# Optimization experiments

Hardware: AMD Instinct MI355X
Metric: run time of the kernel (lower is better)

The kernel has to match this reference:

```python
import jax, jax.numpy as jnp
import numpy as np

NEG_SLOPE = 0.01  # nn.LeakyReLU default used in module

def leaky_relu(x):
    return jnp.where(x >= 0, x, NEG_SLOPE * x)

def setup_inputs() -> dict:
    key = jax.random.key(0)
    k1, k2, k3, k4, k5 = jax.random.split(key, 5)
    B, S, D, H, E = 4, 2048, 1024, 2048, 8
    s_in = 1.0 / np.sqrt(D)
    return {
        "inputs": jax.random.normal(k1, (B, S, D), dtype=jnp.float32),
        "Wg": jax.random.normal(k2, (E, D), dtype=jnp.float32) * s_in,
        "bg": jax.random.normal(k3, (E,), dtype=jnp.float32) * s_in,
        "We": jax.random.normal(k4, (E, H, D), dtype=jnp.float32) * s_in,
        "be": jax.random.normal(k5, (E, H), dtype=jnp.float32) * s_in,
    }

def reference(inputs, Wg, bg, We, be):
    # gate: [B,S,E]
    gate_logits = jnp.einsum('bsd,ed->bse', inputs, Wg) + bg
    gate_probs = jax.nn.softmax(gate_logits, axis=-1)
    # all experts densely: [B,S,E,H]
    expert_out = leaky_relu(jnp.einsum('bsd,ehd->bseh', inputs, We) + be)
    # gate-weighted reduction over experts: [B,S,H]
    weighted = jnp.einsum('bseh,bse->bsh', expert_out, gate_probs)
    return weighted
```

## Files before the change

kernel.cpp:

```cpp
#include <hip/hip_runtime.h>
#include <hip/hip_bf16.h>
#include <math.h>

#define M_TOK 8192
#define N_H   2048
#define K_D   1024
#define N_E   8

typedef __bf16 bf16x8 __attribute__((ext_vector_type(8)));
typedef __bf16 bf16x4 __attribute__((ext_vector_type(4)));
typedef float  f32x4  __attribute__((ext_vector_type(4)));

__device__ inline f32x4 mfma16(bf16x8 a, bf16x8 b, f32x4 c) {
  return __builtin_amdgcn_mfma_f32_16x16x32_bf16(a, b, c, 0, 0, 0);
}

__device__ inline void load16_lds(const void* g, void* l) {
  __builtin_amdgcn_global_load_lds(
      (const __attribute__((address_space(1))) void*)g,
      (__attribute__((address_space(3))) void*)l, 16, 0, 0);
}

__global__ __launch_bounds__(256) void cvt_kernel(const float* __restrict__ src,
                                                  __bf16* __restrict__ dst,
                                                  int n4) {
  int i = blockIdx.x * blockDim.x + threadIdx.x;
  const int stride = gridDim.x * blockDim.x;
  for (; i < n4; i += stride) {
    float4 v = ((const float4*)src)[i];
    bf16x4 o = {(__bf16)v.x, (__bf16)v.y, (__bf16)v.z, (__bf16)v.w};
    *(bf16x4*)(dst + (size_t)i * 4) = o;
  }
}

__global__ __launch_bounds__(256) void gate_kernel(const float* __restrict__ X,
                                                   const float* __restrict__ Wg,
                                                   const float* __restrict__ bg,
                                                   float* __restrict__ gate) {
  const int tid = threadIdx.x;
  const int lane = tid & 63;
  const int wv = tid >> 6;
  const int token = blockIdx.x * 4 + wv;
  const float* xrow = X + (size_t)token * K_D;

  float xr[16];
#pragma unroll
  for (int i = 0; i < 16; ++i) xr[i] = xrow[lane + i * 64];

  float l[N_E];
#pragma unroll
  for (int e = 0; e < N_E; ++e) {
    const float* wrow = Wg + e * K_D;
    float s = 0.f;
#pragma unroll
    for (int i = 0; i < 16; ++i) s += xr[i] * wrow[lane + i * 64];
#pragma unroll
    for (int off = 32; off > 0; off >>= 1) s += __shfl_xor(s, off);
    l[e] = s + bg[e];
  }
  float mx = l[0];
#pragma unroll
  for (int e = 1; e < N_E; ++e) mx = fmaxf(mx, l[e]);
  float p[N_E], den = 0.f;
#pragma unroll
  for (int e = 0; e < N_E; ++e) { p[e] = expf(l[e] - mx); den += p[e]; }
  const float inv = 1.f / den;
  if (lane == 0) {
#pragma unroll
    for (int e = 0; e < N_E; ++e) gate[(size_t)token * N_E + e] = p[e] * inv;
  }
}

__global__ __launch_bounds__(256, 2) void moe_main(
    const __bf16* __restrict__ Xb, const __bf16* __restrict__ Wb,
    const float* __restrict__ gate, const float* __restrict__ be,
    float* __restrict__ out) {
  __shared__ __bf16 As[128 * 32];
  __shared__ __bf16 Bs[128 * 32];
  __shared__ float gS[128 * 8];
  __shared__ float bS[8 * 128];

  const int tid = threadIdx.x;
  const int lane = tid & 63;
  const int wv = tid >> 6;
  const int wr = wv >> 1, wc = wv & 1;
  const int row0 = blockIdx.x * 128;
  const int col0 = blockIdx.y * 128;

  for (int i = tid; i < 1024; i += 256) {
    gS[i] = gate[(size_t)row0 * N_E + i];
    bS[i] = be[(size_t)(i >> 7) * N_H + col0 + (i & 127)];
  }

  const int rA = tid >> 2;
  const int kk = (tid & 3) * 8;
  const __bf16* aP0 = Xb + (size_t)(row0 + rA) * K_D + kk;
  const __bf16* aP1 = aP0 + (size_t)64 * K_D;

  const int lr = lane & 15;
  const int lk = (lane >> 4) * 8;
  const __bf16* aRd = &As[(wr * 64 + lr) * 32 + lk];
  const __bf16* bRd = &Bs[(wc * 64 + lr) * 32 + lk];

  f32x4 fin[4][4];
#pragma unroll
  for (int m = 0; m < 4; ++m)
#pragma unroll
    for (int n = 0; n < 4; ++n) fin[m][n] = (f32x4){0.f, 0.f, 0.f, 0.f};

  for (int e = 0; e < N_E; ++e) {
    const __bf16* bP0 =
        Wb + (size_t)e * N_H * K_D + (size_t)(col0 + rA) * K_D + kk;
    const __bf16* bP1 = bP0 + (size_t)64 * K_D;

    f32x4 acc[4][4];
#pragma unroll
    for (int m = 0; m < 4; ++m)
#pragma unroll
      for (int n = 0; n < 4; ++n) acc[m][n] = (f32x4){0.f, 0.f, 0.f, 0.f};

    for (int kt = 0; kt < K_D / 32; ++kt) {
      const int k0 = kt * 32;
      __syncthreads();
      load16_lds(aP0 + k0, &As[wv * 512]);
      load16_lds(aP1 + k0, &As[2048 + wv * 512]);
      load16_lds(bP0 + k0, &Bs[wv * 512]);
      load16_lds(bP1 + k0, &Bs[2048 + wv * 512]);
      __syncthreads();

      bf16x8 af[4], bfr[4];
#pragma unroll
      for (int m = 0; m < 4; ++m) af[m] = *(const bf16x8*)(aRd + m * 16 * 32);
#pragma unroll
      for (int n = 0; n < 4; ++n) bfr[n] = *(const bf16x8*)(bRd + n * 16 * 32);
#pragma unroll
      for (int m = 0; m < 4; ++m)
#pragma unroll
        for (int n = 0; n < 4; ++n)
          acc[m][n] = mfma16(af[m], bfr[n], acc[m][n]);
    }

#pragma unroll
    for (int m = 0; m < 4; ++m) {
#pragma unroll
      for (int j = 0; j < 4; ++j) {
        const int r = wr * 64 + m * 16 + (lane >> 4) * 4 + j;
        const float g = gS[r * 8 + e];
#pragma unroll
        for (int n = 0; n < 4; ++n) {
          float v = acc[m][n][j] + bS[e * 128 + wc * 64 + n * 16 + lr];
          v = (v >= 0.f) ? v : 0.01f * v;
          fin[m][n][j] += g * v;
        }
      }
    }
  }

#pragma unroll
  for (int m = 0; m < 4; ++m) {
#pragma unroll
    for (int j = 0; j < 4; ++j) {
      const size_t r = (size_t)(row0 + wr * 64 + m * 16 + (lane >> 4) * 4 + j);
#pragma unroll
      for (int n = 0; n < 4; ++n) {
        out[r * N_H + col0 + wc * 64 + n * 16 + lr] = fin[m][n][j];
      }
    }
  }
}

extern "C" void kernel_launch(void* const* d_in, const int* in_sizes, int n_in,
                              void* d_out, int out_size, void* d_ws, size_t ws_size,
                              hipStream_t stream) {
  const float* X  = (const float*)d_in[0];
  const float* Wg = (const float*)d_in[1];
  const float* bg = (const float*)d_in[2];
  const float* We = (const float*)d_in[3];
  const float* be = (const float*)d_in[4];
  float* out = (float*)d_out;

  char* ws = (char*)d_ws;
  __bf16* Xb   = (__bf16*)(ws);
  __bf16* Wb   = (__bf16*)(ws + (size_t)16 * 1024 * 1024);
  float*  gate = (float*)(ws + (size_t)48 * 1024 * 1024);

  cvt_kernel<<<2048, 256, 0, stream>>>(X, Xb, (M_TOK * K_D) / 4);
  cvt_kernel<<<2048, 256, 0, stream>>>(We, Wb, (N_E * N_H * K_D) / 4);

  gate_kernel<<<M_TOK / 4, 256, 0, stream>>>(X, Wg, bg, gate);

  dim3 grid(M_TOK / 128, N_H / 128);
  moe_main<<<grid, 256, 0, stream>>>(Xb, Wb, gate, be, out);
}
```

Before: 367.9 us.

## Process two experts per K-loop pass to reuse A tile and halve barriers

Restructures the expert loop so each K-sweep loads B tiles for two experts at once and computes both against the same A fragments. This halves the number of A tile loads and syncthreads pairs per block and doubles the MFMA work per barrier. In exchange the accumulator grows to 4x8 f32x4 per wave (128 extra VGPRs), which risks spills or lower occupancy under launch_bounds(256,2), and B shared memory doubles.

```diff
diff --git a/kernel.cpp b/kernel.cpp
--- a/kernel.cpp
+++ b/kernel.cpp
@@ -76,14 +76,14 @@
     const float* __restrict__ gate, const float* __restrict__ be,
     float* __restrict__ out) {
   __shared__ __bf16 As[128 * 32];
-  __shared__ __bf16 Bs[128 * 32];
+  __shared__ __bf16 Bs[256 * 32];
   __shared__ float gS[128 * 8];
   __shared__ float bS[8 * 128];
 
   const int tid = threadIdx.x;
   const int lane = tid & 63;
   const int wv = tid >> 6;
-  const int wr = wv >> 1, wc = wv & 1;
+  const int wr = wv >> 1, wn = wv & 1;
   const int row0 = blockIdx.x * 128;
   const int col0 = blockIdx.y * 128;
 
@@ -100,24 +100,27 @@
   const int lr = lane & 15;
   const int lk = (lane >> 4) * 8;
   const __bf16* aRd = &As[(wr * 64 + lr) * 32 + lk];
-  const __bf16* bRd = &Bs[(wc * 64 + lr) * 32 + lk];
+  const __bf16* bRd = &Bs[(wn * 64 + lr) * 32 + lk];
 
   f32x4 fin[4][4];
 #pragma unroll
   for (int m = 0; m < 4; ++m)
 #pragma unroll
-    for (int n = 0; n < 4; ++n) fin[m][n] = (f32x4){0.f, 0.f, 0.f, 0.f};
-
-  for (int e = 0; e < N_E; ++e) {
-    const __bf16* bP0 =
-        Wb + (size_t)e * N_H * K_D + (size_t)(col0 + rA) * K_D + kk;
-    const __bf16* bP1 = bP0 + (size_t)64 * K_D;
-
-    f32x4 acc[4][4];
+    for (int h = 0; h < 4; ++h) fin[m][h] = (f32x4){0.f, 0.f, 0.f, 0.f};
+
+  for (int p = 0; p < 4; ++p) {
+    const int e0 = p * 2;
+
+    const __bf16* bP0 = Wb + ((size_t)(e0 + 0) * N_H + col0 + 0  + rA) * K_D + kk;
+    const __bf16* bP1 = Wb + ((size_t)(e0 + 0) * N_H + col0 + 64 + rA) * K_D + kk;
+    const __bf16* bP2 = Wb + ((size_t)(e0 + 1) * N_H + col0 + 0  + rA) * K_D + kk;
+    const __bf16* bP3 = Wb + ((size_t)(e0 + 1) * N_H + col0 + 64 + rA) * K_D + kk;
+
+    f32x4 acc[4][8];
 #pragma unroll
     for (int m = 0; m < 4; ++m)
 #pragma unroll
-      for (int n = 0; n < 4; ++n) acc[m][n] = (f32x4){0.f, 0.f, 0.f, 0.f};
+      for (int n = 0; n < 8; ++n) acc[m][n] = (f32x4){0.f, 0.f, 0.f, 0.f};
 
     for (int kt = 0; kt < K_D / 32; ++kt) {
       const int k0 = kt * 32;
@@ -126,18 +129,21 @@
       load16_lds(aP1 + k0, &As[2048 + wv * 512]);
       load16_lds(bP0 + k0, &Bs[wv * 512]);
       load16_lds(bP1 + k0, &Bs[2048 + wv * 512]);
+      load16_lds(bP2 + k0, &Bs[4096 + wv * 512]);
+      load16_lds(bP3 + k0, &Bs[6144 + wv * 512]);
       __syncthreads();
 
-      bf16x8 af[4], bfr[4];
+      bf16x8 af[4];
 #pragma unroll
       for (int m = 0; m < 4; ++m) af[m] = *(const bf16x8*)(aRd + m * 16 * 32);
 #pragma unroll
-      for (int n = 0; n < 4; ++n) bfr[n] = *(const bf16x8*)(bRd + n * 16 * 32);
-#pragma unroll
-      for (int m = 0; m < 4; ++m)
-#pragma unroll
-        for (int n = 0; n < 4; ++n)
-          acc[m][n] = mfma16(af[m], bfr[n], acc[m][n]);
+      for (int n = 0; n < 8; ++n) {
+        const bf16x8 bfr =
+            *(const bf16x8*)(bRd + ((n >> 2) * 128 + (n & 3) * 16) * 32);
+#pragma unroll
+        for (int m = 0; m < 4; ++m)
+          acc[m][n] = mfma16(af[m], bfr, acc[m][n]);
+      }
     }
 
 #pragma unroll
@@ -145,12 +151,16 @@
 #pragma unroll
       for (int j = 0; j < 4; ++j) {
         const int r = wr * 64 + m * 16 + (lane >> 4) * 4 + j;
-        const float g = gS[r * 8 + e];
-#pragma unroll
-        for (int n = 0; n < 4; ++n) {
-          float v = acc[m][n][j] + bS[e * 128 + wc * 64 + n * 16 + lr];
-          v = (v >= 0.f) ? v : 0.01f * v;
-          fin[m][n][j] += g * v;
+        const float g0 = gS[r * 8 + e0];
+        const float g1 = gS[r * 8 + e0 + 1];
+#pragma unroll
+        for (int h = 0; h < 4; ++h) {
+          const int c = wn * 64 + h * 16 + lr;
+          float v0 = acc[m][h][j] + bS[e0 * 128 + c];
+          v0 = (v0 >= 0.f) ? v0 : 0.01f * v0;
+          float v1 = acc[m][4 + h][j] + bS[(e0 + 1) * 128 + c];
+          v1 = (v1 >= 0.f) ? v1 : 0.01f * v1;
+          fin[m][h][j] += g0 * v0 + g1 * v1;
         }
       }
     }
@@ -162,8 +172,8 @@
     for (int j = 0; j < 4; ++j) {
       const size_t r = (size_t)(row0 + wr * 64 + m * 16 + (lane >> 4) * 4 + j);
 #pragma unroll
-      for (int n = 0; n < 4; ++n) {
-        out[r * N_H + col0 + wc * 64 + n * 16 + lr] = fin[m][n][j];
+      for (int h = 0; h < 4; ++h) {
+        out[r * N_H + col0 + wn * 64 + h * 16 + lr] = fin[m][h][j];
       }
     }
   }
```

Measured after the change: 331.9 us. 9.8% less time.
